# Performance work log

Measured on AMD Instinct MI355X. Metric: run time of the kernel, lower is better.

Reference implementation:

```python
import jax, jax.numpy as jnp
import numpy as np

I, H, C = 1024, 1024, 1000
B, S = 128, 256


def setup_inputs() -> dict:
    key = jax.random.key(0)
    ks = jax.random.split(key, 7)
    s = 1.0 / np.sqrt(H)
    u = lambda k, shape: jax.random.uniform(k, shape, jnp.float32, -s, s)
    return {
        "x": jax.random.normal(ks[0], (B, S, I), jnp.float32),
        "Wxh": u(ks[1], (4 * H, I)),   # nn.Linear(input, 4H).weight
        "bxh": u(ks[2], (4 * H,)),
        "Whh": u(ks[3], (4 * H, H)),   # nn.Linear(hidden, 4H).weight
        "bhh": u(ks[4], (4 * H,)),
        "Wfc": jax.random.normal(ks[5], (C, H), jnp.float32) / np.sqrt(H),
        "bfc": jnp.zeros((C,), jnp.float32),
    }


def reference(x, Wxh, bxh, Whh, bhh, Wfc, bfc):
    # x: [B, S, I]. Precompute input projection for all timesteps (one big GEMM).
    xW = jnp.einsum("bsi,gi->sbg", x, Wxh) + bxh + bhh  # [S, B, 4H]

    def step(carry, xw_t):
        h, c = carry
        gates = xw_t + h @ Whh.T               # [B, 4H]
        gi, gf, gg, go = jnp.split(gates, 4, axis=1)  # chunk order: i, f, chat, o
        it = jax.nn.sigmoid(gi)
        ft = jax.nn.sigmoid(gf)
        ot = jax.nn.sigmoid(go)
        chat = jnp.tanh(gg)
        c_new = c * ft + it * chat
        h_new = ot * jnp.tanh(c_new)
        return (h_new, c_new), None

    h0 = jnp.zeros((x.shape[0], H), x.dtype)
    c0 = jnp.zeros((x.shape[0], H), x.dtype)
    (h_last, _), _ = jax.lax.scan(step, (h0, c0), xW)
    return h_last @ Wfc.T + bfc  # [B, C]
```

## Files before the change

kernel.cpp:

```cpp
#include <hip/hip_runtime.h>
#include <hip/hip_bf16.h>

typedef __attribute__((ext_vector_type(8))) short short8;
typedef __attribute__((ext_vector_type(4))) float f32x4;
typedef unsigned long long u64;
typedef unsigned int u32;

#define SQLEN 256
#define BATCH 128
#define HID   1024
#define G4    4096
#define NCLS  1000

static __device__ __forceinline__ float sigm(float x){ return 1.0f/(1.0f+__expf(-x)); }
static __device__ __forceinline__ float tanhx(float x){ return 2.0f/(1.0f+__expf(-2.0f*x)) - 1.0f; }
static __device__ __forceinline__ short bf16b(float x){
  __hip_bfloat16 h = __float2bfloat16(x);
  return __builtin_bit_cast(short, h);
}
static __device__ __forceinline__ float bf2f(short s){
  return __bfloat162float(__builtin_bit_cast(__hip_bfloat16, s));
}

__global__ void cast_x_kernel(const float* __restrict__ x, short* __restrict__ xbf){
  int r = blockIdx.x;
  int s = r >> 7, b = r & 127;
  const float* src = x + ((size_t)b*SQLEN + s)*HID;
  short* dst = xbf + (size_t)r*HID;
  int k = threadIdx.x*4;
  float4 v = *(const float4*)(src + k);
  short4 o; o.x=bf16b(v.x); o.y=bf16b(v.y); o.z=bf16b(v.z); o.w=bf16b(v.w);
  *(short4*)(dst + k) = o;
}

__global__ void cast_w_kernel(const float* __restrict__ src, short* __restrict__ dst){
  int i = (blockIdx.x*256 + threadIdx.x)*4;
  float4 v = *(const float4*)(src + i);
  short4 o; o.x=bf16b(v.x); o.y=bf16b(v.y); o.z=bf16b(v.z); o.w=bf16b(v.w);
  *(short4*)(dst + i) = o;
}

__global__ void bias_kernel(const float* __restrict__ a, const float* __restrict__ b,
                            float* __restrict__ o){
  int i = blockIdx.x*256 + threadIdx.x;
  o[i] = a[i] + b[i];
}

__global__ __launch_bounds__(512,2) void gemm_xw_kernel(
    const short* __restrict__ A, const short* __restrict__ B,
    const float* __restrict__ bias, short* __restrict__ C)
{
  __shared__ __align__(16) short As[2][16384];
  __shared__ __align__(16) short Bs[2][16384];
  const int tid  = threadIdx.x;
  const int lane = tid & 63;
  const int wave = tid >> 6;
  const int l15  = lane & 15;
  const int quad = lane >> 4;
  const int swz = (((int)blockIdx.x & 7) << 8) + ((int)blockIdx.x >> 3);
  const int bm = swz >> 4;
  const int bn = swz & 15;
  const size_t r0 = (size_t)bm*256, n0 = (size_t)bn*256;
  const int wmr = wave >> 2;
  const int wnc = wave & 3;

  f32x4 acc[8][4];
  #pragma unroll
  for (int m=0;m<8;++m)
    #pragma unroll
    for (int n=0;n<4;++n) acc[m][n] = (f32x4)0.0f;

  auto stage = [&](int buf, int kt){
    const int k0 = kt*64;
    #pragma unroll
    for (int r=0;r<4;++r){
      const int fa = r*8 + wave, m = fa>>1, kit = fa&1;
      __builtin_amdgcn_global_load_lds(
        (const void*)(A + (r0 + m*16 + l15)*HID + k0 + kit*32 + quad*8),
        (void*)((char*)&As[buf][0] + r*8192 + wave*1024), 16, 0, 0);
    }
    #pragma unroll
    for (int r=0;r<4;++r){
      const int fb = r*8 + wave, n = fb>>1, kit = fb&1;
      __builtin_amdgcn_global_load_lds(
        (const void*)(B + (n0 + n*16 + l15)*HID + k0 + kit*32 + quad*8),
        (void*)((char*)&Bs[buf][0] + r*8192 + wave*1024), 16, 0, 0);
    }
  };
  auto compute = [&](int buf){
    #pragma unroll
    for (int kit=0;kit<2;++kit){
      short8 a[8], b[4];
      #pragma unroll
      for (int m=0;m<8;++m)
        a[m] = *(const short8*)((char*)&As[buf][0]
                                + ((wmr*8 + m)*2 + kit)*1024 + lane*16);
      #pragma unroll
      for (int n=0;n<4;++n)
        b[n] = *(const short8*)((char*)&Bs[buf][0]
                                + ((wnc*4 + n)*2 + kit)*1024 + lane*16);
      #pragma unroll
      for (int m=0;m<8;++m)
        #pragma unroll
        for (int n=0;n<4;++n)
          acc[m][n] = __builtin_amdgcn_mfma_f32_16x16x32_bf16(a[m], b[n], acc[m][n], 0,0,0);
    }
  };

  stage(0, 0);
  stage(1, 1);
  asm volatile("s_waitcnt vmcnt(8)\n\ts_barrier" ::: "memory");

  for (int kt = 0; kt < 16; ++kt){
    compute(kt & 1);
    asm volatile("s_waitcnt lgkmcnt(0)\n\ts_barrier" ::: "memory");
    if (kt + 2 < 16) stage(kt & 1, kt + 2);
    if (kt + 1 < 16){
      if (kt + 2 < 16)
        asm volatile("s_waitcnt vmcnt(8)\n\ts_barrier" ::: "memory");
      else
        asm volatile("s_waitcnt vmcnt(0)\n\ts_barrier" ::: "memory");
    }
  }

  const int s_idx = bm*2 + wmr;
  #pragma unroll
  for (int n=0;n<4;++n){
    int s = (int)n0 + wnc*64 + n*16;
    float bs = bias[s + l15];
    int g = s >> 10, jgi = (s & 1023) >> 4;
    #pragma unroll
    for (int m=0;m<8;++m){
      #pragma unroll
      for (int rg=0; rg<4; ++rg){
        u32 w0 = (u32)(unsigned short)bf16b(acc[m][n][rg] + bs);
        u32 w1 = __shfl_down(w0, 1);
        u32 w2 = __shfl_down(w0, 2);
        u32 w3 = __shfl_down(w0, 3);
        if ((l15 & 3) == 0){
          u64 pk = (u64)w0 | ((u64)w1<<16) | ((u64)w2<<32) | ((u64)w3<<48);
          int b = m*16 + quad*4 + rg;
          *(u64*)(C + (((size_t)s_idx*64 + jgi)*128 + b)*64 + g*16 + l15) = pk;
        }
      }
    }
  }
}

__global__ __launch_bounds__(256,2) void lstm_kernel(
    const short* __restrict__ whh, const short* __restrict__ xw,
    short* __restrict__ h_all, u32* __restrict__ flags)
{
  __shared__ f32x4 part[2][4][4][64];

  const int tid  = threadIdx.x;
  const int lane = tid & 63;
  const int wave = tid >> 6;
  const int l15  = lane & 15;
  const int quad = lane >> 4;
  const int bg = blockIdx.x & 7;
  const int jg = blockIdx.x >> 3;
  const int b0 = bg*16;
  const int j0 = jg*16;
  const int ks0 = wave*256;

  __builtin_amdgcn_fence(__ATOMIC_ACQUIRE, "agent");

  short8 Bf[4][8];
  #pragma unroll
  for (int g=0; g<4; ++g)
    #pragma unroll
    for (int kit=0; kit<8; ++kit)
      Bf[g][kit] = *(const short8*)(whh + (size_t)(g*1024 + j0 + l15)*HID
                                    + ks0 + kit*32 + quad*8);

  u32* fgrp = flags + bg*64;

  const int r  = tid >> 4;
  const int jj = tid & 15;
  const int ln = (r>>2)*16 + jj;
  const int rg = r & 3;
  float cc = 0.0f;

  short xwc[4];
  {
    const short* xb = xw + (((size_t)0*64 + jg)*128 + b0 + r)*64 + jj;
    #pragma unroll
    for (int g=0; g<4; ++g) xwc[g] = xb[g*16];
  }

  for (int t = 0; t < SQLEN; ++t){
    const short* hin  = h_all + (size_t)t*131072;
    short*       hout = h_all + (size_t)(t+1)*131072;

    short xwn[4];
    if (t < SQLEN-1){
      const short* xb = xw + (((size_t)(t+1)*64 + jg)*128 + b0 + r)*64 + jj;
      #pragma unroll
      for (int g=0; g<4; ++g) xwn[g] = xb[g*16];
    }

    if (t){
      u32* fp = fgrp + wave*16 + l15;
      while (__hip_atomic_load(fp, __ATOMIC_RELAXED,
                               __HIP_MEMORY_SCOPE_AGENT) < (u32)t)
        __builtin_amdgcn_s_sleep(1);
      asm volatile("" ::: "memory");
    }

    short8 Af[8];
    #pragma unroll
    for (int kit=0; kit<8; ++kit)
      Af[kit] = *(const short8*)(hin + (size_t)(b0 + l15)*HID
                                 + ks0 + kit*32 + quad*8);

    f32x4 acc[4];
    #pragma unroll
    for (int g=0; g<4; ++g) acc[g] = (f32x4)0.0f;
    #pragma unroll
    for (int kit=0; kit<8; ++kit)
      #pragma unroll
      for (int g=0; g<4; ++g)
        acc[g] = __builtin_amdgcn_mfma_f32_16x16x32_bf16(Af[kit], Bf[g][kit], acc[g],0,0,0);

    const int pb = t & 1;
    #pragma unroll
    for (int g=0; g<4; ++g) part[pb][wave][g][lane] = acc[g];
    __syncthreads();

    float gv[4];
    #pragma unroll
    for (int g=0; g<4; ++g){
      float s = bf2f(xwc[g]);
      #pragma unroll
      for (int w=0; w<4; ++w)
        s += ((const float*)&part[pb][w][g][ln])[rg];
      gv[g] = s;
    }

    float it = sigm(gv[0]), ft = sigm(gv[1]), ch = tanhx(gv[2]), ot = sigm(gv[3]);
    cc = cc*ft + it*ch;
    float hv = ot * tanhx(cc);

    u32 w0 = (u32)(unsigned short)bf16b(hv);
    u32 w1 = __shfl_down(w0, 1);
    u32 w2 = __shfl_down(w0, 2);
    u32 w3 = __shfl_down(w0, 3);
    if (!(tid & 3)){
      u64 hp = (u64)w0 | ((u64)w1<<16) | ((u64)w2<<32) | ((u64)w3<<48);
      __hip_atomic_store((u64*)(hout + (size_t)(b0 + r)*HID + j0 + jj), hp,
                         __ATOMIC_RELAXED, __HIP_MEMORY_SCOPE_AGENT);
    }
    xwc[0]=xwn[0]; xwc[1]=xwn[1]; xwc[2]=xwn[2]; xwc[3]=xwn[3];
    __syncthreads();

    if (t < SQLEN-1 && tid == 0)
      __hip_atomic_store(fgrp + jg, (u32)(t+1), __ATOMIC_RELAXED,
                         __HIP_MEMORY_SCOPE_AGENT);
  }
}

__global__ __launch_bounds__(256) void fc_kernel(const short* __restrict__ h,
    const float* __restrict__ wfc, const float* __restrict__ bfc, float* __restrict__ out)
{
  __shared__ float hs[4][1024];
  int tid = threadIdx.x;
  int b0 = (blockIdx.x >> 3)*4;
  int cs = (blockIdx.x & 7)*125;
  for (int i = tid; i < 4096; i += 256){
    int bb = i >> 10, k = i & 1023;
    hs[bb][k] = bf2f(h[(size_t)(b0+bb)*HID + k]);
  }
  __syncthreads();
  for (int c = cs + tid; c < cs + 125; c += 256){
    const float* w = wfc + (size_t)c*HID;
    float a0=0.f,a1=0.f,a2=0.f,a3=0.f;
    for (int k=0; k<1024; k+=4){
      float4 wv = *(const float4*)(w + k);
      a0 += wv.x*hs[0][k] + wv.y*hs[0][k+1] + wv.z*hs[0][k+2] + wv.w*hs[0][k+3];
      a1 += wv.x*hs[1][k] + wv.y*hs[1][k+1] + wv.z*hs[1][k+2] + wv.w*hs[1][k+3];
      a2 += wv.x*hs[2][k] + wv.y*hs[2][k+1] + wv.z*hs[2][k+2] + wv.w*hs[2][k+3];
      a3 += wv.x*hs[3][k] + wv.y*hs[3][k+1] + wv.z*hs[3][k+2] + wv.w*hs[3][k+3];
    }
    float bb = bfc[c];
    out[(size_t)(b0+0)*NCLS + c] = a0 + bb;
    out[(size_t)(b0+1)*NCLS + c] = a1 + bb;
    out[(size_t)(b0+2)*NCLS + c] = a2 + bb;
    out[(size_t)(b0+3)*NCLS + c] = a3 + bb;
  }
}

extern "C" void kernel_launch(void* const* d_in, const int* in_sizes, int n_in,
                              void* d_out, int out_size, void* d_ws, size_t ws_size,
                              hipStream_t stream) {
  const float* x   = (const float*)d_in[0];
  const float* Wxh = (const float*)d_in[1];
  const float* bxh = (const float*)d_in[2];
  const float* Whh = (const float*)d_in[3];
  const float* bhh = (const float*)d_in[4];
  const float* Wfc = (const float*)d_in[5];
  const float* bfc = (const float*)d_in[6];
  float* out = (float*)d_out;

  char* ws = (char*)d_ws;
  short*    h_all = (short*)(ws + 0);
  short*    xbf   = (short*)(ws + 0);
  short*    wxhb  = (short*)(ws + 68157440);
  short*    whhb  = (short*)(ws + 76546048);
  float*    biasg = (float*)(ws + 84934656);
  short*    xw    = (short*)(ws + 85983232);
  u32*      flags = (u32*)(ws + 354418688);

  hipMemsetAsync(flags, 0, 4096, stream);

  cast_x_kernel<<<32768, 256, 0, stream>>>(x, xbf);
  cast_w_kernel<<<4096, 256, 0, stream>>>(Wxh, wxhb);
  cast_w_kernel<<<4096, 256, 0, stream>>>(Whh, whhb);
  bias_kernel  <<<16,   256, 0, stream>>>(bxh, bhh, biasg);
  gemm_xw_kernel<<<2048, 512, 0, stream>>>(xbf, wxhb, biasg, xw);
  hipMemsetAsync(ws, 0, 262144, stream);
  lstm_kernel  <<<512,  256, 0, stream>>>(whhb, xw, h_all, flags);
  fc_kernel    <<<256,  256, 0, stream>>>(h_all + (size_t)SQLEN*131072, Wfc, bfc, out);
}
```

Measured before the change: 1.648 ms.

## Interleave half-tile LDS prefetch with MFMA phases in input-projection GEMM

The input-projection GEMM main loop moves from a two-stage, whole-tile stage/compute scheme to a finer schedule. The loop is split into four phases per k-tile, and each phase issues a slice of the next A/B global-to-LDS loads between LDS reads and MFMA bursts. It also raises wave priority with s_setprio around the MFMA bursts and uses tuned vmcnt waits. The goal is to hide global-load latency and cut barrier stalls, at the cost of more barriers and a fragile hand-counted wait sequence.

```diff
diff --git a/kernel.cpp b/kernel.cpp
--- a/kernel.cpp
+++ b/kernel.cpp
@@ -70,58 +70,104 @@
     #pragma unroll
     for (int n=0;n<4;++n) acc[m][n] = (f32x4)0.0f;
 
-  auto stage = [&](int buf, int kt){
-    const int k0 = kt*64;
-    #pragma unroll
-    for (int r=0;r<4;++r){
-      const int fa = r*8 + wave, m = fa>>1, kit = fa&1;
+  auto stageA = [&](int buf, int j, int kit){
+    const int k0 = j*64 + kit*32;
+    #pragma unroll
+    for (int i=0;i<2;++i){
+      const int m = wave*2 + i;
       __builtin_amdgcn_global_load_lds(
-        (const void*)(A + (r0 + m*16 + l15)*HID + k0 + kit*32 + quad*8),
-        (void*)((char*)&As[buf][0] + r*8192 + wave*1024), 16, 0, 0);
-    }
-    #pragma unroll
-    for (int r=0;r<4;++r){
-      const int fb = r*8 + wave, n = fb>>1, kit = fb&1;
+        (const void*)(A + (r0 + m*16 + l15)*HID + k0 + quad*8),
+        (void*)((char*)&As[buf][0] + (m*2+kit)*1024), 16, 0, 0);
+    }
+  };
+  auto stageB = [&](int buf, int j, int kit){
+    const int k0 = j*64 + kit*32;
+    #pragma unroll
+    for (int i=0;i<2;++i){
+      const int n = wave*2 + i;
       __builtin_amdgcn_global_load_lds(
-        (const void*)(B + (n0 + n*16 + l15)*HID + k0 + kit*32 + quad*8),
-        (void*)((char*)&Bs[buf][0] + r*8192 + wave*1024), 16, 0, 0);
+        (const void*)(B + (n0 + n*16 + l15)*HID + k0 + quad*8),
+        (void*)((char*)&Bs[buf][0] + (n*2+kit)*1024), 16, 0, 0);
     }
   };
-  auto compute = [&](int buf){
-    #pragma unroll
-    for (int kit=0;kit<2;++kit){
-      short8 a[8], b[4];
-      #pragma unroll
-      for (int m=0;m<8;++m)
-        a[m] = *(const short8*)((char*)&As[buf][0]
-                                + ((wmr*8 + m)*2 + kit)*1024 + lane*16);
-      #pragma unroll
-      for (int n=0;n<4;++n)
-        b[n] = *(const short8*)((char*)&Bs[buf][0]
-                                + ((wnc*4 + n)*2 + kit)*1024 + lane*16);
-      #pragma unroll
-      for (int m=0;m<8;++m)
+
+  #define BAR  asm volatile("s_barrier" ::: "memory")
+
+  stageB(0,0,0); stageA(0,0,0); stageB(0,0,1); stageA(0,0,1);
+  stageB(1,1,0); stageA(1,1,0); stageB(1,1,1);
+  asm volatile("s_waitcnt vmcnt(10)" ::: "memory");
+  BAR;
+
+  #pragma unroll 1
+  for (int kt = 0; kt < 16; ++kt){
+    const int buf = kt & 1;
+    char* Ab = (char*)&As[buf][0];
+    char* Bb = (char*)&Bs[buf][0];
+    {
+      short8 a[4], b[4], a2[4];
+      #pragma unroll
+      for (int i=0;i<4;++i) a[i] = *(const short8*)(Ab + ((wmr*8+i)*2+0)*1024 + lane*16);
+      #pragma unroll
+      for (int j=0;j<4;++j) b[j] = *(const short8*)(Bb + ((wnc*4+j)*2+0)*1024 + lane*16);
+      if (kt+1 < 16) stageA((kt+1)&1, kt+1, 1);
+      BAR;
+      __builtin_amdgcn_s_setprio(1);
+      #pragma unroll
+      for (int i=0;i<4;++i)
         #pragma unroll
-        for (int n=0;n<4;++n)
-          acc[m][n] = __builtin_amdgcn_mfma_f32_16x16x32_bf16(a[m], b[n], acc[m][n], 0,0,0);
-    }
-  };
-
-  stage(0, 0);
-  stage(1, 1);
-  asm volatile("s_waitcnt vmcnt(8)\n\ts_barrier" ::: "memory");
-
-  for (int kt = 0; kt < 16; ++kt){
-    compute(kt & 1);
-    asm volatile("s_waitcnt lgkmcnt(0)\n\ts_barrier" ::: "memory");
-    if (kt + 2 < 16) stage(kt & 1, kt + 2);
-    if (kt + 1 < 16){
-      if (kt + 2 < 16)
-        asm volatile("s_waitcnt vmcnt(8)\n\ts_barrier" ::: "memory");
-      else
-        asm volatile("s_waitcnt vmcnt(0)\n\ts_barrier" ::: "memory");
-    }
-  }
+        for (int j=0;j<4;++j)
+          acc[i][j] = __builtin_amdgcn_mfma_f32_16x16x32_bf16(a[i], b[j], acc[i][j], 0,0,0);
+      __builtin_amdgcn_s_setprio(0);
+      BAR;
+      #pragma unroll
+      for (int i=0;i<4;++i) a2[i] = *(const short8*)(Ab + ((wmr*8+4+i)*2+0)*1024 + lane*16);
+      if (kt+2 < 16) stageB(buf, kt+2, 0);
+      BAR;
+      __builtin_amdgcn_s_setprio(1);
+      #pragma unroll
+      for (int i=0;i<4;++i)
+        #pragma unroll
+        for (int j=0;j<4;++j)
+          acc[4+i][j] = __builtin_amdgcn_mfma_f32_16x16x32_bf16(a2[i], b[j], acc[4+i][j], 0,0,0);
+      __builtin_amdgcn_s_setprio(0);
+      if (kt <= 13)      asm volatile("s_waitcnt vmcnt(10)" ::: "memory");
+      else if (kt == 14) asm volatile("s_waitcnt vmcnt(8)"  ::: "memory");
+      else               asm volatile("s_waitcnt vmcnt(0)"  ::: "memory");
+      BAR;
+    }
+    {
+      short8 a[4], b[4], a2[4];
+      #pragma unroll
+      for (int i=0;i<4;++i) a[i] = *(const short8*)(Ab + ((wmr*8+i)*2+1)*1024 + lane*16);
+      #pragma unroll
+      for (int j=0;j<4;++j) b[j] = *(const short8*)(Bb + ((wnc*4+j)*2+1)*1024 + lane*16);
+      if (kt+2 < 16) stageA(buf, kt+2, 0);
+      BAR;
+      __builtin_amdgcn_s_setprio(1);
+      #pragma unroll
+      for (int i=0;i<4;++i)
+        #pragma unroll
+        for (int j=0;j<4;++j)
+          acc[i][j] = __builtin_amdgcn_mfma_f32_16x16x32_bf16(a[i], b[j], acc[i][j], 0,0,0);
+      __builtin_amdgcn_s_setprio(0);
+      BAR;
+      #pragma unroll
+      for (int i=0;i<4;++i) a2[i] = *(const short8*)(Ab + ((wmr*8+4+i)*2+1)*1024 + lane*16);
+      if (kt+2 < 16) stageB(buf, kt+2, 1);
+      BAR;
+      __builtin_amdgcn_s_setprio(1);
+      #pragma unroll
+      for (int i=0;i<4;++i)
+        #pragma unroll
+        for (int j=0;j<4;++j)
+          acc[4+i][j] = __builtin_amdgcn_mfma_f32_16x16x32_bf16(a2[i], b[j], acc[4+i][j], 0,0,0);
+      __builtin_amdgcn_s_setprio(0);
+      if (kt <= 13)      asm volatile("s_waitcnt vmcnt(10)" ::: "memory");
+      else if (kt == 14) asm volatile("s_waitcnt vmcnt(4)"  ::: "memory");
+      BAR;
+    }
+  }
+  #undef BAR
 
   const int s_idx = bm*2 + wmr;
   #pragma unroll
```

After: 1.603 ms. 2.8% less time.
